# Performance work log

Measured on AMD Instinct MI355X. Metric: run time of the kernel, lower is better.

## Reference

```python
import jax, jax.numpy as jnp
import numpy as np
from jax import lax

B, L, DIM = 2, 2048, 2048
HK, HV = 16, 32
DK, DV = 128, 128
KCONV = 4
KEY_DIM = HK * DK          # 2048
VAL_DIM = HV * DV          # 4096
CONV_DIM = 2 * KEY_DIM + VAL_DIM  # 8192
EPS = 1e-6


def _l2norm(x, eps=1e-6):
    return x * lax.rsqrt((x * x).sum(-1, keepdims=True) + eps)


def _gated_delta_rule(q, k, v, g, beta):
    # q,k: (B,L,H,DK); v: (B,L,H,DV); g,beta: (B,L,H)
    q = _l2norm(q.astype(jnp.float32)) * (DK ** -0.5)
    k = _l2norm(k.astype(jnp.float32))
    v = v.astype(jnp.float32)
    g = g.astype(jnp.float32)
    beta = beta.astype(jnp.float32)
    # time-major for scan: (L,B,H,...)
    qs = q.transpose(1, 0, 2, 3)
    ks = k.transpose(1, 0, 2, 3)
    vs = v.transpose(1, 0, 2, 3)
    gs = g.transpose(1, 0, 2)
    bs = beta.transpose(1, 0, 2)
    state0 = jnp.zeros((B, HV, DK, DV), jnp.float32)

    def step(state, inp):
        q_t, k_t, v_t, g_t, b_t = inp
        state = state * jnp.exp(g_t)[..., None, None]          # decay
        kv_mem = jnp.einsum('bhk,bhkv->bhv', k_t, state)       # read
        delta = (v_t - kv_mem) * b_t[..., None]                # error-correct
        state = state + jnp.einsum('bhk,bhv->bhkv', k_t, delta)
        out_t = jnp.einsum('bhk,bhkv->bhv', q_t, state)
        return state, out_t

    _, outs = lax.scan(step, state0, (qs, ks, vs, gs, bs))
    return outs.transpose(1, 0, 2, 3)  # (B,L,H,DV)


def setup_inputs() -> dict:
    key = jax.random.key(0)
    ks = jax.random.split(key, 8)
    s = 0.02
    return {
        'x': jax.random.normal(ks[0], (B, L, DIM), jnp.float32),
        'W_qkv': jax.random.normal(ks[1], (CONV_DIM, DIM), jnp.float32) * s,
        'W_z': jax.random.normal(ks[2], (VAL_DIM, DIM), jnp.float32) * s,
        'W_a': jax.random.normal(ks[3], (HV, DIM), jnp.float32) * s,
        'W_b': jax.random.normal(ks[4], (HV, DIM), jnp.float32) * s,
        'conv_w': jax.random.normal(ks[5], (CONV_DIM, 1, KCONV), jnp.float32) * 0.2,
        'A_log': jnp.log(jax.random.uniform(ks[6], (HV,), jnp.float32, 1e-6, 16.0)),
        'dt_bias': jnp.ones((HV,), jnp.float32),
        'norm_weight': jnp.ones((DV,), jnp.float32),
        'W_out': jax.random.normal(ks[7], (DIM, VAL_DIM), jnp.float32) * s,
    }


def reference(x, W_qkv, W_z, W_a, W_b, conv_w, A_log, dt_bias, norm_weight, W_out):
    qkv = x @ W_qkv.T                      # (B,L,CONV_DIM)
    z = x @ W_z.T                          # (B,L,VAL_DIM)
    a = x @ W_a.T                          # (B,L,HV)
    b = x @ W_b.T                          # (B,L,HV)
    # depthwise causal conv1d (left pad K-1)
    h = qkv.transpose(0, 2, 1)             # (B,C,L)
    h = lax.conv_general_dilated(h, conv_w, window_strides=(1,),
                                 padding=[(KCONV - 1, 0)],
                                 dimension_numbers=('NCH', 'OIH', 'NCH'),
                                 feature_group_count=CONV_DIM)
    qkv = jax.nn.silu(h.transpose(0, 2, 1))
    q, k, v = jnp.split(qkv, [KEY_DIM, 2 * KEY_DIM], axis=-1)
    q = q.reshape(B, L, HK, DK)
    k = k.reshape(B, L, HK, DK)
    v = v.reshape(B, L, HV, DV)
    rep = HV // HK
    if rep > 1:
        q = jnp.repeat(q, rep, axis=2)
        k = jnp.repeat(k, rep, axis=2)
    g = -jnp.exp(A_log.astype(jnp.float32)) * jax.nn.softplus(a.astype(jnp.float32) + dt_bias)
    beta = jax.nn.sigmoid(b)
    out = _gated_delta_rule(q, k, v, g, beta)   # (B,L,HV,DV) fp32
    # gated RMSNorm over DV: silu(z) * weight * norm(out)
    var = (out * out).mean(-1, keepdims=True)
    out = out * lax.rsqrt(var + EPS) * norm_weight
    zg = z.reshape(B, L, HV, DV)
    out = out * jax.nn.silu(zg.astype(jnp.float32))
    out = out.astype(x.dtype).reshape(B, L, VAL_DIM)
    return out @ W_out.T
```

## Files before the change

### kernel.cpp

```cpp
#include <hip/hip_runtime.h>
#include <hip/hip_bf16.h>
#include <cstddef>
#include <cstdint>

constexpr int B = 2, L = 2048, DIM = 2048;
constexpr int HK = 16, HV = 32, DK = 128, DV = 128;
constexpr int KEY_DIM = HK * DK;
constexpr int VAL_DIM = HV * DV;
constexpr int CONV_DIM = 2 * KEY_DIM + VAL_DIM;
constexpr int NPROJ = CONV_DIM + VAL_DIM + HV + HV;
constexpr int NPAD  = ((NPROJ + 255) / 256) * 256;
constexpr size_t ROWS = (size_t)B * L;
constexpr float EPS = 1e-6f;
constexpr int CHUNK = 64, NCHUNK = L / CHUNK;
constexpr int NCH_TOT = B * HV * NCHUNK;
constexpr int CONV_LT = 8;
constexpr int CONV_TL = L / CONV_LT;

constexpr size_t OFF_QKV  = 0;
constexpr size_t OFF_Z    = OFF_QKV + ROWS * CONV_DIM * 2;
constexpr size_t OFF_A    = OFF_Z   + ROWS * VAL_DIM * 2;
constexpr size_t OFF_B    = OFF_A   + ROWS * HV * 4;
constexpr size_t OFF_G    = OFF_B   + ROWS * HV * 4;
constexpr size_t OFF_BETA = OFF_G   + ROWS * HV * 4;
constexpr size_t OFF_U    = OFF_BETA + ROWS * HV * 4;
constexpr size_t OFF_WQK  = OFF_U + (size_t)NCH_TOT * CHUNK * DV * 4;
constexpr size_t OFF_HALO = OFF_WQK + (size_t)NCH_TOT * CHUNK * CHUNK * 2;
constexpr size_t WS_NEED_BYTES = OFF_HALO + (size_t)3 * B * CONV_LT * CONV_DIM * 2;
constexpr size_t OFF_WCAT = OFF_U;
constexpr size_t OFF_XB   = OFF_WQK;
constexpr size_t OFF_WOB  = OFF_U;
static_assert((size_t)NPAD * DIM * 2 <= (size_t)NCH_TOT * CHUNK * DV * 4, "Wcat fits U");

__device__ __forceinline__ float bf2f(unsigned short u) {
    union { float f; uint32_t i; } c; c.i = ((uint32_t)u) << 16; return c.f;
}
__device__ __forceinline__ unsigned short f2bf(float f) {
    union { float f; uint32_t u; } c; c.f = f;
    uint32_t u = c.u + 0x7FFFu + ((c.u >> 16) & 1u);
    return (unsigned short)(u >> 16);
}
__device__ __forceinline__ uint32_t pk2(float a, float b) {
    return (uint32_t)f2bf(a) | ((uint32_t)f2bf(b) << 16);
}

typedef __attribute__((ext_vector_type(8))) short bfrag;
typedef __attribute__((ext_vector_type(4))) float ffrag;

__device__ __forceinline__ void gload16(const unsigned short* g, unsigned short* l) {
    __builtin_amdgcn_global_load_lds(
        (const __attribute__((address_space(1))) uint32_t*)g,
        (__attribute__((address_space(3))) uint32_t*)l, 16, 0, 0);
}

__device__ __forceinline__ const float* w_row_multi(int n, const float* Wq, const float* Wz,
                                                    const float* Wa, const float* Wb) {
    if (n < CONV_DIM)                return Wq + (size_t)n * DIM;
    if (n < CONV_DIM + VAL_DIM)      return Wz + (size_t)(n - CONV_DIM) * DIM;
    if (n < CONV_DIM + VAL_DIM + HV) return Wa + (size_t)(n - CONV_DIM - VAL_DIM) * DIM;
    return Wb + (size_t)(n - CONV_DIM - VAL_DIM - HV) * DIM;
}

__global__ __launch_bounds__(256) void cvt_wcat(
    const float* __restrict__ Wq, const float* __restrict__ Wz,
    const float* __restrict__ Wa, const float* __restrict__ Wb,
    unsigned short* __restrict__ dst)
{
    const int r = blockIdx.x;
    const int c = threadIdx.x * 8;
    uint4 o;
    if (r < NPROJ) {
        const float* s = w_row_multi(r, Wq, Wz, Wa, Wb) + c;
        float4 v0 = *(const float4*)s;
        float4 v1 = *(const float4*)(s + 4);
        o = make_uint4(pk2(v0.x, v0.y), pk2(v0.z, v0.w), pk2(v1.x, v1.y), pk2(v1.z, v1.w));
    } else {
        o = make_uint4(0u, 0u, 0u, 0u);
    }
    *(uint4*)&dst[(size_t)r * DIM + c] = o;
}

__global__ __launch_bounds__(256) void cvt_f32bf(const float* __restrict__ src,
                                                 unsigned short* __restrict__ dst, int cols)
{
    const size_t r = blockIdx.x;
    for (int c = threadIdx.x * 8; c < cols; c += 256 * 8) {
        const float* s = src + r * cols + c;
        float4 v0 = *(const float4*)s;
        float4 v1 = *(const float4*)(s + 4);
        *(uint4*)&dst[r * cols + c] =
            make_uint4(pk2(v0.x, v0.y), pk2(v0.z, v0.w), pk2(v1.x, v1.y), pk2(v1.z, v1.w));
    }
}

__device__ __forceinline__ void store_multi(int m, int n, float v,
                                            unsigned short* qkv, unsigned short* z,
                                            float* a, float* b) {
    if (n < CONV_DIM) {
        qkv[(size_t)m * CONV_DIM + n] = f2bf(v);
    } else if (n < CONV_DIM + VAL_DIM) {
        z[(size_t)m * VAL_DIM + (n - CONV_DIM)] = f2bf(v);
    } else if (n < CONV_DIM + VAL_DIM + HV) {
        a[(size_t)m * HV + (n - CONV_DIM - VAL_DIM)] = v;
    } else if (n < NPROJ) {
        b[(size_t)m * HV + (n - CONV_DIM - VAL_DIM - HV)] = v;
    }
}

constexpr int BK = 64;

constexpr int GBUF2 = 16384;
constexpr int GEMM_SMEM = 2 * GBUF2 * 2;

__global__ __launch_bounds__(256) void gemm_inproj_bf(
    const unsigned short* __restrict__ xb,
    const unsigned short* __restrict__ Wcat,
    unsigned short* __restrict__ qkv, unsigned short* __restrict__ z,
    float* __restrict__ a_out, float* __restrict__ b_out)
{
    extern __shared__ __align__(16) unsigned short lds[];

    constexpr int NT  = DIM / BK;
    constexpr int NBY = (int)ROWS / 128;
    constexpr int NBX = NPAD / 128;
    constexpr int NB  = NBY * NBX;
    const int id  = blockIdx.x;
    const int swz = (id & 7) * (NB >> 3) + (id >> 3);
    const int by  = swz & 31;
    const int bx  = swz >> 5;
    const int row0 = by * 128;
    const int col0 = bx * 128;

    const int t = threadIdx.x, lane = t & 63, wid = t >> 6;
    const int wm = (wid >> 1) * 64, wn = (wid & 1) * 64;
    const int quad = lane >> 4, l16 = lane & 15;
    const int x7 = l16 & 7;

    ffrag acc[4][4];
#pragma unroll
    for (int i = 0; i < 4; ++i)
#pragma unroll
        for (int j = 0; j < 4; ++j) acc[i][j] = (ffrag)0.f;

    const int srow = t >> 3;
    const int scol = (((t & 7) ^ (srow & 7)) * 8);
    const unsigned short* aS = xb   + (size_t)(row0 + srow) * DIM + scol;
    const unsigned short* bS = Wcat + (size_t)(col0 + srow) * DIM + scol;
    unsigned short* aD0 = lds + (wid * 8) * 64;
    unsigned short* bD0 = lds + 8192 + (wid * 8) * 64;

    auto STAGE = [&](int kt) {
        const int b = kt & 1;
        unsigned short* aD = aD0 + b * GBUF2;
        unsigned short* bD = bD0 + b * GBUF2;
        const int k0 = kt * BK;
#pragma unroll
        for (int g = 0; g < 4; ++g) {
            gload16(aS + (size_t)(g * 32) * DIM + k0, aD + g * 32 * 64);
            gload16(bS + (size_t)(g * 32) * DIM + k0, bD + g * 32 * 64);
        }
    };

    auto COMPUTE = [&](int kt) {
        const int b = kt & 1;
        const unsigned short* A  = lds + b * GBUF2;
        const unsigned short* Bm = lds + b * GBUF2 + 8192;
#pragma unroll
        for (int kk = 0; kk < 2; ++kk) {
            const int so = ((kk * 4 + quad) ^ x7) * 8;
            bfrag aF[4], bF[4];
#pragma unroll
            for (int m = 0; m < 4; ++m)
                aF[m] = *(const bfrag*)&A[(wm + m * 16 + l16) * 64 + so];
#pragma unroll
            for (int n = 0; n < 4; ++n)
                bF[n] = *(const bfrag*)&Bm[(wn + n * 16 + l16) * 64 + so];
            __builtin_amdgcn_s_setprio(1);
#pragma unroll
            for (int m = 0; m < 4; ++m)
#pragma unroll
                for (int n = 0; n < 4; ++n)
                    acc[m][n] = __builtin_amdgcn_mfma_f32_16x16x32_bf16(
                        aF[m], bF[n], acc[m][n], 0, 0, 0);
            __builtin_amdgcn_s_setprio(0);
        }
    };

    STAGE(0); STAGE(1);
    asm volatile("s_waitcnt vmcnt(8)" ::: "memory");
    asm volatile("s_barrier" ::: "memory");
    for (int kt = 0; kt < NT; ++kt) {
        COMPUTE(kt);
        if (kt == NT - 1) break;
        asm volatile("s_barrier" ::: "memory");
        if (kt + 2 < NT) {
            STAGE(kt + 2);
            asm volatile("s_waitcnt vmcnt(8)" ::: "memory");
        } else {
            asm volatile("s_waitcnt vmcnt(0)" ::: "memory");
        }
        asm volatile("s_barrier" ::: "memory");
    }

#pragma unroll
    for (int m = 0; m < 4; ++m)
#pragma unroll
        for (int n = 0; n < 4; ++n) {
            int gr = row0 + wm + m * 16 + quad * 4;
            int gc = col0 + wn + n * 16 + l16;
#pragma unroll
            for (int reg = 0; reg < 4; ++reg)
                store_multi(gr + reg, gc, acc[m][n][reg], qkv, z, a_out, b_out);
        }
}

constexpr int GBUF3 = 24576;
constexpr int GEMM3_SMEM = 3 * GBUF3 * 2;

__global__ __launch_bounds__(512, 1) void gemm_outproj_bf(
    const unsigned short* __restrict__ A,
    const unsigned short* __restrict__ Wb,
    float* __restrict__ C)
{
    extern __shared__ __align__(16) unsigned short lds[];

    constexpr int NT  = VAL_DIM / BK;
    constexpr int NBY = (int)ROWS / 256;
    constexpr int NBX = DIM / 128;
    constexpr int NB  = NBY * NBX;
    const int id  = blockIdx.x;
    const int swz = (id & 7) * (NB >> 3) + (id >> 3);
    const int by  = swz & 15;
    const int bx  = swz >> 4;
    const int row0 = by * 256;
    const int col0 = bx * 128;

    const int t = threadIdx.x, lane = t & 63, wid = t >> 6;
    const int wr = wid >> 1, wc = wid & 1;
    const int quad = lane >> 4, l16 = lane & 15;
    const int x7 = l16 & 7;

    ffrag acc[4][4];
#pragma unroll
    for (int i = 0; i < 4; ++i)
#pragma unroll
        for (int j = 0; j < 4; ++j) acc[i][j] = (ffrag)0.f;

    const int srow = t >> 3;
    const int scol = (((t & 7) ^ (srow & 7)) * 8);
    const unsigned short* aS = A  + (size_t)(row0 + srow) * VAL_DIM + scol;
    const unsigned short* bS = Wb + (size_t)(col0 + srow) * VAL_DIM + scol;
    unsigned short* aD0 = lds + (wid * 8) * 64;
    unsigned short* bD0 = lds + 16384 + (wid * 8) * 64;

    auto STAGE = [&](int kt) {
        const int b = kt % 3;
        unsigned short* aD = aD0 + b * GBUF3;
        unsigned short* bD = bD0 + b * GBUF3;
        const int k0 = kt * BK;
#pragma unroll
        for (int g = 0; g < 4; ++g)
            gload16(aS + (size_t)(g * 64) * VAL_DIM + k0, aD + g * 64 * 64);
#pragma unroll
        for (int g = 0; g < 2; ++g)
            gload16(bS + (size_t)(g * 64) * VAL_DIM + k0, bD + g * 64 * 64);
    };

    auto COMPUTE = [&](int kt) {
        const int b = kt % 3;
        const unsigned short* Am = lds + b * GBUF3;
        const unsigned short* Bm = lds + b * GBUF3 + 16384;
#pragma unroll
        for (int kk = 0; kk < 2; ++kk) {
            const int so = ((kk * 4 + quad) ^ x7) * 8;
            bfrag aF[4], bF[4];
#pragma unroll
            for (int m = 0; m < 4; ++m)
                aF[m] = *(const bfrag*)&Am[(wr * 64 + m * 16 + l16) * 64 + so];
#pragma unroll
            for (int n = 0; n < 4; ++n)
                bF[n] = *(const bfrag*)&Bm[(wc * 64 + n * 16 + l16) * 64 + so];
#pragma unroll
            for (int m = 0; m < 4; ++m)
#pragma unroll
                for (int n = 0; n < 4; ++n)
                    acc[m][n] = __builtin_amdgcn_mfma_f32_16x16x32_bf16(
                        aF[m], bF[n], acc[m][n], 0, 0, 0);
        }
    };

    STAGE(0); STAGE(1);
    asm volatile("s_waitcnt vmcnt(6)" ::: "memory");
    asm volatile("s_barrier" ::: "memory");
    for (int kt = 0; kt < NT; ++kt) {
        if (kt + 2 < NT) {
            STAGE(kt + 2);
            asm volatile("s_waitcnt vmcnt(12)" ::: "memory");
        } else if (kt + 1 < NT) {
            asm volatile("s_waitcnt vmcnt(6)" ::: "memory");
        } else {
            asm volatile("s_waitcnt vmcnt(0)" ::: "memory");
        }
        asm volatile("s_barrier" ::: "memory");
        COMPUTE(kt);
        asm volatile("s_barrier" ::: "memory");
    }

#pragma unroll
    for (int m = 0; m < 4; ++m)
#pragma unroll
        for (int n = 0; n < 4; ++n) {
            int gr = row0 + wr * 64 + m * 16 + quad * 4;
            int gc = col0 + wc * 64 + n * 16 + l16;
#pragma unroll
            for (int reg = 0; reg < 4; ++reg)
                C[(size_t)(gr + reg) * DIM + gc] = acc[m][n][reg];
        }
}

__global__ __launch_bounds__(256) void conv_halo(const unsigned short* __restrict__ qkv,
                                                 unsigned short* __restrict__ hbuf)
{
    int idx = blockIdx.x * 256 + threadIdx.x;
    int c    = idx & (CONV_DIM - 1);
    int tile = (idx >> 13) & (CONV_LT - 1);
    int b    = idx >> 16;
    int l0 = tile * CONV_TL;
    const unsigned short* p = qkv + (size_t)b * L * CONV_DIM + c;
#pragma unroll
    for (int j = 0; j < 3; ++j) {
        unsigned short v = (tile > 0) ? p[(size_t)(l0 - 3 + j) * CONV_DIM] : (unsigned short)0;
        hbuf[((size_t)j * B * CONV_LT + b * CONV_LT + tile) * CONV_DIM + c] = v;
    }
}

__global__ __launch_bounds__(256) void conv_silu(unsigned short* __restrict__ qkv,
                                                 const float* __restrict__ conv_w,
                                                 const unsigned short* __restrict__ hbuf)
{
    int idx = blockIdx.x * 256 + threadIdx.x;
    int c    = idx & (CONV_DIM - 1);
    int tile = (idx >> 13) & (CONV_LT - 1);
    int b    = idx >> 16;
    const float w0 = conv_w[c * 4 + 0];
    const float w1 = conv_w[c * 4 + 1];
    const float w2 = conv_w[c * 4 + 2];
    const float w3 = conv_w[c * 4 + 3];
    unsigned short* p = qkv + ((size_t)b * L + tile * CONV_TL) * CONV_DIM + c;
    const size_t hb = (size_t)b * CONV_LT + tile;
    float x0 = bf2f(hbuf[((size_t)0 * B * CONV_LT + hb) * CONV_DIM + c]);
    float x1 = bf2f(hbuf[((size_t)1 * B * CONV_LT + hb) * CONV_DIM + c]);
    float x2 = bf2f(hbuf[((size_t)2 * B * CONV_LT + hb) * CONV_DIM + c]);
    for (int l0 = 0; l0 < CONV_TL; l0 += 8) {
        float xv[8];
#pragma unroll
        for (int j = 0; j < 8; ++j) xv[j] = bf2f(p[(size_t)(l0 + j) * CONV_DIM]);
#pragma unroll
        for (int j = 0; j < 8; ++j) {
            float h = w0 * x0 + w1 * x1 + w2 * x2 + w3 * xv[j];
            float s = h / (1.f + __expf(-h));
            p[(size_t)(l0 + j) * CONV_DIM] = f2bf(s);
            x0 = x1; x1 = x2; x2 = xv[j];
        }
    }
}

__global__ __launch_bounds__(256) void normqk(unsigned short* __restrict__ qkv)
{
    int wid  = blockIdx.x * 4 + (threadIdx.x >> 6);
    int lane = threadIdx.x & 63;
    int hk  = wid & 15;
    int sel = (wid >> 4) & 1;
    int row = wid >> 5;
    unsigned short* p = qkv + (size_t)row * CONV_DIM + sel * KEY_DIM + hk * DK;
    float x0 = bf2f(p[lane]), x1 = bf2f(p[lane + 64]);
    float ss = x0 * x0 + x1 * x1;
#pragma unroll
    for (int o = 32; o >= 1; o >>= 1) ss += __shfl_xor(ss, o);
    float sc = rsqrtf(ss + 1e-6f);
    if (sel == 0) sc *= 0.08838834764831845f;
    p[lane]      = f2bf(x0 * sc);
    p[lane + 64] = f2bf(x1 * sc);
}

__global__ __launch_bounds__(256) void gatecoef(const float* __restrict__ a_buf,
                                                const float* __restrict__ b_buf,
                                                const float* __restrict__ A_log,
                                                const float* __restrict__ dt_bias,
                                                float* __restrict__ glog,
                                                float* __restrict__ beta)
{
    int idx = blockIdx.x * blockDim.x + threadIdx.x;
    int h = idx & (HV - 1);
    float av = a_buf[idx];
    float bv = b_buf[idx];
    float x  = av + dt_bias[h];
    float sp = (x > 20.f) ? x : log1pf(__expf(x));
    glog[idx] = -__expf(A_log[h]) * sp;
    beta[idx] = 1.f / (1.f + __expf(-bv));
}


constexpr int RSK  = 136;
constexpr int RST  = 72;
constexpr int RSTD = 68;
constexpr int RSR1 = 260;

constexpr int P1_oKs  = 0;
constexpr int P1_oQs  = P1_oKs + 64 * RSK * 2;
constexpr int P1_oDT  = 0;
constexpr int P1_oAf  = P1_oQs + 64 * RSK * 2;
constexpr int P1_oRHS = P1_oAf + 64 * RST * 2;
constexpr int P1_oG   = P1_oRHS + 64 * RSR1 * 4;
constexpr int P1_oEG  = P1_oG + 256;
constexpr int P1_oBs  = P1_oEG + 256;
constexpr int P1_SMEM = P1_oBs + 256;

__global__ __launch_bounds__(256, 1) void chunk_prep(
    unsigned short* __restrict__ qkv,
    const float* __restrict__ glog,
    const float* __restrict__ beta,
    float* __restrict__ Ubuf,
    unsigned short* __restrict__ Wqkbuf)
{
    extern __shared__ __align__(16) char smem[];
    unsigned short* sKs = (unsigned short*)(smem + P1_oKs);
    unsigned short* sQs = (unsigned short*)(smem + P1_oQs);
    unsigned short* sDT = (unsigned short*)(smem + P1_oDT);
    unsigned short* sAf = (unsigned short*)(smem + P1_oAf);
    float* sRHS = (float*)(smem + P1_oRHS);
    float* sG   = (float*)(smem + P1_oG);
    float* sEG  = (float*)(smem + P1_oEG);
    float* sBs  = (float*)(smem + P1_oBs);

    const int bid = blockIdx.x;
    const int ch = bid & (NCHUNK - 1);
    const int h  = (bid >> 5) & (HV - 1);
    const int bb = bid >> 10;
    const int hk = h >> 1;
    const int t    = threadIdx.x;
    const int w    = t >> 6;
    const int lane = t & 63;
    const int quad = lane >> 4;
    const int l16  = lane & 15;
    const int quad8 = quad * 8;
    const size_t bL = (size_t)bb * L;
    const int l0 = ch * CHUNK;
    const int VOFF = 2 * KEY_DIM + h * DV;

    {
        const int r  = t >> 2;
        const int c0 = (t & 3) * 32;
        const unsigned short* grow = qkv + (bL + l0 + r) * CONV_DIM;
        const unsigned short* gq = grow + hk * DK + c0;
        const unsigned short* gk = grow + KEY_DIM + hk * DK + c0;
#pragma unroll
        for (int u = 0; u < 4; ++u) {
            *(uint4*)&sKs[r * RSK + c0 + 8 * u] = *(const uint4*)(gk + 8 * u);
            *(uint4*)&sQs[r * RSK + c0 + 8 * u] = *(const uint4*)(gq + 8 * u);
        }
        if (t < 64) {
            float gl = glog[(bL + l0 + t) * HV + h];
#pragma unroll
            for (int off = 1; off < 64; off <<= 1) {
                float v = __shfl_up(gl, off, 64);
                if (lane >= off) gl += v;
            }
            sG[t]  = gl;
            sEG[t] = __expf(gl);
            sBs[t] = beta[(bL + l0 + t) * HV + h];
        }
    }
    __syncthreads();

    {
        ffrag accA[4], accW[4];
#pragma unroll
        for (int mt = 0; mt < 4; ++mt) { accA[mt] = (ffrag)0.f; accW[mt] = (ffrag)0.f; }
#pragma unroll
        for (int kk = 0; kk < 4; ++kk) {
            bfrag bf = *(const bfrag*)&sKs[(16 * w + l16) * RSK + 32 * kk + quad8];
#pragma unroll
            for (int mt = 0; mt < 4; ++mt) {
                bfrag ak = *(const bfrag*)&sKs[(16 * mt + l16) * RSK + 32 * kk + quad8];
                bfrag aq = *(const bfrag*)&sQs[(16 * mt + l16) * RSK + 32 * kk + quad8];
                accA[mt] = __builtin_amdgcn_mfma_f32_16x16x32_bf16(ak, bf, accA[mt], 0, 0, 0);
                accW[mt] = __builtin_amdgcn_mfma_f32_16x16x32_bf16(aq, bf, accW[mt], 0, 0, 0);
            }
        }
        const int j = 16 * w + l16;
        const float gj = sG[j];
        unsigned short* Wqp = Wqkbuf + (size_t)bid * (CHUNK * CHUNK);
#pragma unroll
        for (int mt = 0; mt < 4; ++mt)
#pragma unroll
            for (int reg = 0; reg < 4; ++reg) {
                int i = 16 * mt + quad * 4 + reg;
                float sc = __expf(sG[i] - gj);
                sAf[i * RST + j] = f2bf((j < i) ? sBs[i] * sc * accA[mt][reg] : 0.f);
                Wqp[i * CHUNK + j] = f2bf((j <= i) ? sc * accW[mt][reg] : 0.f);
            }
    }

    {
        const int r  = t >> 2;
        const int c0 = (t & 3) * 32;
        const float be  = sBs[r];
        const float beg = be * sEG[r];
        const unsigned short* gv = qkv + (bL + l0 + r) * CONV_DIM + VOFF + c0;
#pragma unroll
        for (int u = 0; u < 4; ++u) {
            uint4 vv = *(const uint4*)(gv + 8 * u);
            const unsigned short* vp = (const unsigned short*)&vv;
#pragma unroll
            for (int e = 0; e < 8; ++e)
                sRHS[r * RSR1 + c0 + 8 * u + e] = be * bf2f(vp[e]);
        }
#pragma unroll
        for (int u = 0; u < 4; ++u)
#pragma unroll
            for (int e = 0; e < 8; ++e)
                sRHS[r * RSR1 + 128 + c0 + 8 * u + e] =
                    beg * bf2f(sKs[r * RSK + c0 + 8 * u + e]);
    }
    __syncthreads();

    for (int u = t; u < 256 * RSTD / 2; u += 256) ((uint32_t*)sDT)[u] = 0;

    float* Up = Ubuf + (size_t)bid * (CHUNK * DV);
    for (int sb = 0; sb < 4; ++sb) {
        const int sb16 = 16 * sb;
        if (sb > 0) {
            const int kbn = (sb + 1) >> 1;
            ffrag c16[4];
#pragma unroll
            for (int nt = 0; nt < 4; ++nt) c16[nt] = (ffrag)0.f;
            for (int kb = 0; kb < kbn; ++kb) {
                bfrag af = *(const bfrag*)&sAf[(sb16 + l16) * RST + 32 * kb + quad8];
#pragma unroll
                for (int nt = 0; nt < 4; ++nt) {
                    bfrag bf = *(const bfrag*)&sDT[(64 * w + 16 * nt + l16) * RSTD + 32 * kb + quad8];
                    c16[nt] = __builtin_amdgcn_mfma_f32_16x16x32_bf16(af, bf, c16[nt], 0, 0, 0);
                }
            }
#pragma unroll
            for (int nt = 0; nt < 4; ++nt)
#pragma unroll
                for (int reg = 0; reg < 4; ++reg)
                    sRHS[(sb16 + quad * 4 + reg) * RSR1 + 64 * w + 16 * nt + l16] -= c16[nt][reg];
        }
        __syncthreads();
        {
            const int c = t;
            float d16[16];
#pragma unroll
            for (int e = 0; e < 16; ++e) {
                const int i = sb16 + e;
                float acc = sRHS[i * RSR1 + c];
#pragma unroll
                for (int f = 0; f < 16; ++f)
                    if (f < e) acc -= bf2f(sAf[i * RST + sb16 + f]) * d16[f];
                d16[e] = acc;
            }
#pragma unroll
            for (int e = 0; e < 16; e += 2)
                *(uint32_t*)&sDT[c * RSTD + sb16 + e] = pk2(d16[e], d16[e + 1]);
            if (c < 128) {
                float* up = Up + c;
#pragma unroll
                for (int e = 0; e < 16; ++e) up[(size_t)(sb16 + e) * DV] = d16[e];
            } else {
                unsigned short* wp = qkv + (bL + l0 + sb16) * CONV_DIM + VOFF + (c - 128);
#pragma unroll
                for (int e = 0; e < 16; ++e) wp[(size_t)e * CONV_DIM] = f2bf(-d16[e]);
            }
        }
        __syncthreads();
    }
}

constexpr int S3_oKT  = 0;
constexpr int S3_oQs  = S3_oKT + 128 * RST * 2;
constexpr int S3_oWk  = S3_oQs + 64 * RSK * 2;
constexpr int S3_oWqk = S3_oWk + 64 * RSK * 2;
constexpr int S3_oSTb = S3_oWqk + 64 * RST * 2;
constexpr int S3_oDT  = S3_oSTb + 32 * RSK * 2;
constexpr int S3_oDdT = S3_oDT + 32 * RST * 2;
constexpr int S3_oEG  = S3_oDdT + 32 * RST * 2;
constexpr int S3_oEGd = S3_oEG + 256;
constexpr int S3_SMEM = S3_oEGd + 256;

__global__ __launch_bounds__(256, 1) void chunk_scan3(
    const unsigned short* __restrict__ qkv,
    const float* __restrict__ glog,
    float* __restrict__ Ubuf,
    const unsigned short* __restrict__ Wqkbuf)
{
    extern __shared__ __align__(16) char smem[];
    unsigned short* sKT  = (unsigned short*)(smem + S3_oKT);
    unsigned short* sQs  = (unsigned short*)(smem + S3_oQs);
    unsigned short* sWk  = (unsigned short*)(smem + S3_oWk);
    unsigned short* sWqk = (unsigned short*)(smem + S3_oWqk);
    unsigned short* sSTb = (unsigned short*)(smem + S3_oSTb);
    unsigned short* sDT  = (unsigned short*)(smem + S3_oDT);
    unsigned short* sDdT = (unsigned short*)(smem + S3_oDdT);
    float* sEG  = (float*)(smem + S3_oEG);
    float* sEGd = (float*)(smem + S3_oEGd);

    const int g  = blockIdx.x & 3;
    const int bh = blockIdx.x >> 2;
    const int h  = bh & (HV - 1);
    const int bb = bh >> 5;
    const int hk = h >> 1;
    const int DV0 = g * 32;
    const int t    = threadIdx.x;
    const int w    = t >> 6;
    const int lane = t & 63;
    const int quad = lane >> 4;
    const int l16  = lane & 15;
    const int quad8 = quad * 8;
    const size_t bL = (size_t)bb * L;
    const int VOFF = 2 * KEY_DIM + h * DV;
    const size_t chbase0 = ((size_t)bb * HV + h) * NCHUNK;

    const int r  = t >> 2;
    const int c0 = (t & 3) * 32;
    const int cw = (t & 3) * 16;

    ffrag accS[2][2];
#pragma unroll
    for (int m = 0; m < 2; ++m)
#pragma unroll
        for (int n = 0; n < 2; ++n) accS[m][n] = (ffrag)0.f;

    for (int u = t; u < 32 * RSK / 2; u += 256) ((uint32_t*)sSTb)[u] = 0;

    uint4 pQ[4], pK[4], pWk[4], pWqk2[2];
    float pGl;

    auto PF = [&](int ch) {
        const int l0p = ch * CHUNK;
        const unsigned short* grow = qkv + (bL + l0p + r) * CONV_DIM;
        const unsigned short* gq = grow + hk * DK + c0;
        const unsigned short* gk = grow + KEY_DIM + hk * DK + c0;
        const unsigned short* gw = grow + VOFF + c0;
#pragma unroll
        for (int u = 0; u < 4; ++u) {
            pQ[u]  = *(const uint4*)(gq + 8 * u);
            pK[u]  = *(const uint4*)(gk + 8 * u);
            pWk[u] = *(const uint4*)(gw + 8 * u);
        }
        const unsigned short* qp = Wqkbuf + (chbase0 + ch) * (CHUNK * CHUNK) + r * CHUNK + cw;
        pWqk2[0] = *(const uint4*)qp;
        pWqk2[1] = *(const uint4*)(qp + 8);
        pGl = glog[(bL + l0p + (t & 63)) * HV + h];
    };

    PF(0);

    for (int ch = 0; ch < NCHUNK; ++ch) {
        const size_t cb = chbase0 + ch;
        float* Uch = Ubuf + cb * (CHUNK * DV);
        __syncthreads();

        ffrag accD[2];
        {
            const float* up = Uch + (size_t)(16 * w + quad * 4) * DV + DV0 + l16;
#pragma unroll
            for (int nt = 0; nt < 2; ++nt)
#pragma unroll
                for (int reg = 0; reg < 4; ++reg)
                    accD[nt][reg] = up[(size_t)reg * DV + 16 * nt];
        }

#pragma unroll
        for (int u = 0; u < 4; ++u) {
            *(uint4*)&sQs[r * RSK + c0 + 8 * u] = pQ[u];
            *(uint4*)&sWk[r * RSK + c0 + 8 * u] = pWk[u];
            const unsigned short* kp = (const unsigned short*)&pK[u];
#pragma unroll
            for (int e = 0; e < 8; ++e) {
                const int c = c0 + 8 * u + e;
                sKT[c * RST + ((((r >> 3) ^ (c >> 3)) & 7) << 3) + (r & 7)] = kp[e];
            }
        }
        *(uint4*)&sWqk[r * RST + cw]     = pWqk2[0];
        *(uint4*)&sWqk[r * RST + cw + 8] = pWqk2[1];

        {
            float gl = pGl;
            if (t < 64) {
#pragma unroll
                for (int off = 1; off < 64; off <<= 1) {
                    float v = __shfl_up(gl, off, 64);
                    if (lane >= off) gl += v;
                }
                float gc = __shfl(gl, 63, 64);
                sEG[t]  = __expf(gl);
                sEGd[t] = __expf(gc - gl);
            }
        }

        if (ch + 1 < NCHUNK) PF(ch + 1);
        __syncthreads();

#pragma unroll
        for (int kk = 0; kk < 4; ++kk) {
            bfrag af = *(const bfrag*)&sWk[(16 * w + l16) * RSK + 32 * kk + quad8];
#pragma unroll
            for (int nt = 0; nt < 2; ++nt) {
                bfrag bf = *(const bfrag*)&sSTb[(16 * nt + l16) * RSK + 32 * kk + quad8];
                accD[nt] = __builtin_amdgcn_mfma_f32_16x16x32_bf16(af, bf, accD[nt], 0, 0, 0);
            }
        }

        {
            const int i0 = 16 * w + quad * 4;
            const float e0 = sEGd[i0], e1 = sEGd[i0 + 1], e2 = sEGd[i0 + 2], e3 = sEGd[i0 + 3];
#pragma unroll
            for (int nt = 0; nt < 2; ++nt) {
                const int dv = 16 * nt + l16;
                const float d0 = accD[nt][0], d1 = accD[nt][1];
                const float d2 = accD[nt][2], d3 = accD[nt][3];
                *(uint32_t*)&sDT[dv * RST + i0]      = pk2(d0, d1);
                *(uint32_t*)&sDT[dv * RST + i0 + 2]  = pk2(d2, d3);
                *(uint32_t*)&sDdT[dv * RST + i0]     = pk2(d0 * e0, d1 * e1);
                *(uint32_t*)&sDdT[dv * RST + i0 + 2] = pk2(d2 * e2, d3 * e3);
            }
        }
        __syncthreads();

        ffrag accO[2];
#pragma unroll
        for (int nt = 0; nt < 2; ++nt) accO[nt] = (ffrag)0.f;
#pragma unroll
        for (int kk = 0; kk < 4; ++kk) {
            bfrag af = *(const bfrag*)&sQs[(16 * w + l16) * RSK + 32 * kk + quad8];
#pragma unroll
            for (int nt = 0; nt < 2; ++nt) {
                bfrag bf = *(const bfrag*)&sSTb[(16 * nt + l16) * RSK + 32 * kk + quad8];
                accO[nt] = __builtin_amdgcn_mfma_f32_16x16x32_bf16(af, bf, accO[nt], 0, 0, 0);
            }
        }
#pragma unroll
        for (int nt = 0; nt < 2; ++nt)
#pragma unroll
            for (int reg = 0; reg < 4; ++reg)
                accO[nt][reg] *= sEG[16 * w + quad * 4 + reg];
#pragma unroll
        for (int kk = 0; kk < 2; ++kk) {
            bfrag af = *(const bfrag*)&sWqk[(16 * w + l16) * RST + 32 * kk + quad8];
#pragma unroll
            for (int nt = 0; nt < 2; ++nt) {
                bfrag bf = *(const bfrag*)&sDT[(16 * nt + l16) * RST + 32 * kk + quad8];
                accO[nt] = __builtin_amdgcn_mfma_f32_16x16x32_bf16(af, bf, accO[nt], 0, 0, 0);
            }
        }
        {
            float* op = Uch + (size_t)(16 * w + quad * 4) * DV + DV0 + l16;
#pragma unroll
            for (int nt = 0; nt < 2; ++nt)
#pragma unroll
                for (int reg = 0; reg < 4; ++reg)
                    op[(size_t)reg * DV + 16 * nt] = accO[nt][reg];
        }

        {
            const float eGc = sEG[63];
#pragma unroll
            for (int m = 0; m < 2; ++m)
#pragma unroll
                for (int n = 0; n < 2; ++n)
#pragma unroll
                    for (int reg = 0; reg < 4; ++reg) accS[m][n][reg] *= eGc;
#pragma unroll
            for (int kk = 0; kk < 2; ++kk) {
#pragma unroll
                for (int m = 0; m < 2; ++m) {
                    bfrag a0 = *(const bfrag*)&sDdT[(16 * m + l16) * RST + 32 * kk + quad8];
#pragma unroll
                    for (int n = 0; n < 2; ++n) {
                        const int ck = 32 * w + 16 * n + l16;
                        bfrag bk = *(const bfrag*)&sKT[ck * RST +
                                     ((((4 * kk + quad) ^ (ck >> 3)) & 7) << 3)];
                        accS[m][n] = __builtin_amdgcn_mfma_f32_16x16x32_bf16(a0, bk, accS[m][n], 0, 0, 0);
                    }
                }
            }
        }
        __syncthreads();

#pragma unroll
        for (int m = 0; m < 2; ++m)
#pragma unroll
            for (int n = 0; n < 2; ++n)
#pragma unroll
                for (int reg = 0; reg < 4; ++reg)
                    sSTb[(16 * m + quad * 4 + reg) * RSK + 32 * w + 16 * n + l16] =
                        f2bf(accS[m][n][reg]);
    }
}

__global__ __launch_bounds__(256) void rmsgate(
    const float* __restrict__ Obuf,
    unsigned short* __restrict__ z_io,
    const float* __restrict__ norm_w)
{
    const int gw   = blockIdx.x * 4 + (threadIdx.x >> 6);
    const int lane = threadIdx.x & 63;
    const int h  = gw & (HV - 1);
    const int lg = gw >> 5;
    const int bb = lg >> 11;
    const int l  = lg & (L - 1);
    const int ch = l >> 6, i = l & 63;
    const size_t cb = ((size_t)bb * HV + h) * NCHUNK + ch;
    const int dv0 = lane * 2;

    float2 o = *(const float2*)(Obuf + cb * (CHUNK * DV) + (size_t)i * DV + dv0);
    float p = o.x * o.x + o.y * o.y;
#pragma unroll
    for (int m = 1; m < 64; m <<= 1) p += __shfl_xor(p, m, 64);
    float inv = rsqrtf(p * (1.f / 128.f) + EPS);

    unsigned short* zp = z_io + ((size_t)bb * L + l) * VAL_DIM + h * DV + dv0;
    uint32_t zu = *(const uint32_t*)zp;
    float z0 = bf2f((unsigned short)(zu & 0xFFFF));
    float z1 = bf2f((unsigned short)(zu >> 16));
    float y0 = o.x * inv * norm_w[dv0]     * (z0 / (1.f + __expf(-z0)));
    float y1 = o.y * inv * norm_w[dv0 + 1] * (z1 / (1.f + __expf(-z1)));
    *(uint32_t*)zp = pk2(y0, y1);
}

extern "C" void kernel_launch(void* const* d_in, const int* in_sizes, int n_in,
                              void* d_out, int out_size, void* d_ws, size_t ws_size,
                              hipStream_t stream)
{
    const float* x        = (const float*)d_in[0];
    const float* W_qkv    = (const float*)d_in[1];
    const float* W_z      = (const float*)d_in[2];
    const float* W_a      = (const float*)d_in[3];
    const float* W_b      = (const float*)d_in[4];
    const float* conv_w   = (const float*)d_in[5];
    const float* A_log    = (const float*)d_in[6];
    const float* dt_bias  = (const float*)d_in[7];
    const float* norm_w   = (const float*)d_in[8];
    const float* W_out    = (const float*)d_in[9];
    float* out = (float*)d_out;
    char*  ws  = (char*)d_ws;

    if (ws_size < WS_NEED_BYTES) return;

    unsigned short* qkv = (unsigned short*)(ws + OFF_QKV);
    unsigned short* z   = (unsigned short*)(ws + OFF_Z);
    float* a    = (float*)(ws + OFF_A);
    float* bbuf = (float*)(ws + OFF_B);
    float* gl   = (float*)(ws + OFF_G);
    float* beta = (float*)(ws + OFF_BETA);
    float* Ubuf = (float*)(ws + OFF_U);
    unsigned short* Wqkbuf = (unsigned short*)(ws + OFF_WQK);
    unsigned short* hbuf   = (unsigned short*)(ws + OFF_HALO);
    unsigned short* Wcat   = (unsigned short*)(ws + OFF_WCAT);
    unsigned short* xb     = (unsigned short*)(ws + OFF_XB);
    unsigned short* Wob    = (unsigned short*)(ws + OFF_WOB);

    static bool attr_set = false;
    if (!attr_set) {
        (void)hipFuncSetAttribute((const void*)chunk_prep,
                                  hipFuncAttributeMaxDynamicSharedMemorySize, P1_SMEM);
        (void)hipFuncSetAttribute((const void*)chunk_scan3,
                                  hipFuncAttributeMaxDynamicSharedMemorySize, S3_SMEM);
        (void)hipFuncSetAttribute((const void*)gemm_inproj_bf,
                                  hipFuncAttributeMaxDynamicSharedMemorySize, GEMM_SMEM);
        (void)hipFuncSetAttribute((const void*)gemm_outproj_bf,
                                  hipFuncAttributeMaxDynamicSharedMemorySize, GEMM3_SMEM);
        attr_set = true;
    }

    cvt_wcat<<<NPAD, 256, 0, stream>>>(W_qkv, W_z, W_a, W_b, Wcat);
    cvt_f32bf<<<(int)ROWS, 256, 0, stream>>>(x, xb, DIM);
    gemm_inproj_bf<<<((int)ROWS / 128) * (NPAD / 128), 256, GEMM_SMEM, stream>>>(
        xb, Wcat, qkv, z, a, bbuf);
    conv_halo<<<(B * CONV_LT * CONV_DIM) / 256, 256, 0, stream>>>(qkv, hbuf);
    conv_silu<<<(B * CONV_LT * CONV_DIM) / 256, 256, 0, stream>>>(qkv, conv_w, hbuf);
    normqk<<<(B * L * 2 * HK) / 4, 256, 0, stream>>>(qkv);
    gatecoef<<<(B * L * HV) / 256, 256, 0, stream>>>(a, bbuf, A_log, dt_bias, gl, beta);
    chunk_prep<<<NCH_TOT, 256, P1_SMEM, stream>>>(qkv, gl, beta, Ubuf, Wqkbuf);
    chunk_scan3<<<B * HV * 4, 256, S3_SMEM, stream>>>(qkv, gl, Ubuf, Wqkbuf);
    rmsgate<<<(int)(ROWS * HV) / 4, 256, 0, stream>>>(Ubuf, z, norm_w);
    cvt_f32bf<<<DIM, 256, 0, stream>>>(W_out, Wob, VAL_DIM);
    gemm_outproj_bf<<<((int)ROWS / 256) * (DIM / 128), 512, GEMM3_SMEM, stream>>>(z, Wob, out);
}
```

Baseline: 880.8 us.

## Shrink GEMM K-tile to 32 and retile out-projection to 128x128 blocks

Both projection GEMMs now use a 32-wide K tile with a double-buffered 32 KB LDS footprint and a new 4-way XOR swizzle. The out-projection drops from 256x128 tiles with 512 threads and triple buffering to 128x128 tiles with 256 threads, matching the in-projection pipeline. The smaller LDS use should let more blocks reside per CU for better latency hiding and give more blocks for the out-projection. In exchange there are twice as many K iterations and barriers, and each tile gets less data reuse.

```diff
diff --git a/kernel.cpp b/kernel.cpp
--- a/kernel.cpp
+++ b/kernel.cpp
@@ -107,10 +107,10 @@
     }
 }
 
-constexpr int BK = 64;
-
-constexpr int GBUF2 = 16384;
-constexpr int GEMM_SMEM = 2 * GBUF2 * 2;
+constexpr int BK32  = 32;
+constexpr int GBUFA = 4096;
+constexpr int GBUFP = 8192;
+constexpr int GEMM_SMEM32 = 2 * GBUFP * 2;
 
 __global__ __launch_bounds__(256) void gemm_inproj_bf(
     const unsigned short* __restrict__ xb,
@@ -120,7 +120,7 @@
 {
     extern __shared__ __align__(16) unsigned short lds[];
 
-    constexpr int NT  = DIM / BK;
+    constexpr int NT  = DIM / BK32;
     constexpr int NBY = (int)ROWS / 128;
     constexpr int NBX = NPAD / 128;
     constexpr int NB  = NBY * NBX;
@@ -134,7 +134,6 @@
     const int t = threadIdx.x, lane = t & 63, wid = t >> 6;
     const int wm = (wid >> 1) * 64, wn = (wid & 1) * 64;
     const int quad = lane >> 4, l16 = lane & 15;
-    const int x7 = l16 & 7;
 
     ffrag acc[4][4];
 #pragma unroll
@@ -142,52 +141,50 @@
 #pragma unroll
         for (int j = 0; j < 4; ++j) acc[i][j] = (ffrag)0.f;
 
-    const int srow = t >> 3;
-    const int scol = (((t & 7) ^ (srow & 7)) * 8);
-    const unsigned short* aS = xb   + (size_t)(row0 + srow) * DIM + scol;
-    const unsigned short* bS = Wcat + (size_t)(col0 + srow) * DIM + scol;
-    unsigned short* aD0 = lds + (wid * 8) * 64;
-    unsigned short* bD0 = lds + 8192 + (wid * 8) * 64;
+    const int srow = wid * 32 + (lane >> 2);
+    const int scol = (((lane & 3) ^ ((lane >> 2) & 3)) * 8);
+    const unsigned short* aS0 = xb   + (size_t)(row0 + srow) * DIM + scol;
+    const unsigned short* aS1 = aS0 + (size_t)16 * DIM;
+    const unsigned short* bS0 = Wcat + (size_t)(col0 + srow) * DIM + scol;
+    const unsigned short* bS1 = bS0 + (size_t)16 * DIM;
+    unsigned short* aD = lds + wid * 1024;
+    unsigned short* bD = lds + GBUFA + wid * 1024;
 
     auto STAGE = [&](int kt) {
         const int b = kt & 1;
-        unsigned short* aD = aD0 + b * GBUF2;
-        unsigned short* bD = bD0 + b * GBUF2;
-        const int k0 = kt * BK;
-#pragma unroll
-        for (int g = 0; g < 4; ++g) {
-            gload16(aS + (size_t)(g * 32) * DIM + k0, aD + g * 32 * 64);
-            gload16(bS + (size_t)(g * 32) * DIM + k0, bD + g * 32 * 64);
-        }
+        const int k0 = kt * BK32;
+        unsigned short* a  = aD + b * GBUFP;
+        unsigned short* bb = bD + b * GBUFP;
+        gload16(aS0 + k0, a);
+        gload16(aS1 + k0, a + 512);
+        gload16(bS0 + k0, bb);
+        gload16(bS1 + k0, bb + 512);
     };
 
     auto COMPUTE = [&](int kt) {
         const int b = kt & 1;
-        const unsigned short* A  = lds + b * GBUF2;
-        const unsigned short* Bm = lds + b * GBUF2 + 8192;
-#pragma unroll
-        for (int kk = 0; kk < 2; ++kk) {
-            const int so = ((kk * 4 + quad) ^ x7) * 8;
-            bfrag aF[4], bF[4];
-#pragma unroll
-            for (int m = 0; m < 4; ++m)
-                aF[m] = *(const bfrag*)&A[(wm + m * 16 + l16) * 64 + so];
+        const unsigned short* A  = lds + b * GBUFP;
+        const unsigned short* Bm = A + GBUFA;
+        const int so = ((quad ^ (l16 & 3)) << 3);
+        bfrag aF[4], bF[4];
+#pragma unroll
+        for (int m = 0; m < 4; ++m)
+            aF[m] = *(const bfrag*)&A[(wm + m * 16 + l16) * 32 + so];
+#pragma unroll
+        for (int n = 0; n < 4; ++n)
+            bF[n] = *(const bfrag*)&Bm[(wn + n * 16 + l16) * 32 + so];
+        __builtin_amdgcn_s_setprio(1);
+#pragma unroll
+        for (int m = 0; m < 4; ++m)
 #pragma unroll
             for (int n = 0; n < 4; ++n)
-                bF[n] = *(const bfrag*)&Bm[(wn + n * 16 + l16) * 64 + so];
-            __builtin_amdgcn_s_setprio(1);
-#pragma unroll
-            for (int m = 0; m < 4; ++m)
-#pragma unroll
-                for (int n = 0; n < 4; ++n)
-                    acc[m][n] = __builtin_amdgcn_mfma_f32_16x16x32_bf16(
-                        aF[m], bF[n], acc[m][n], 0, 0, 0);
-            __builtin_amdgcn_s_setprio(0);
-        }
+                acc[m][n] = __builtin_amdgcn_mfma_f32_16x16x32_bf16(
+                    aF[m], bF[n], acc[m][n], 0, 0, 0);
+        __builtin_amdgcn_s_setprio(0);
     };
 
     STAGE(0); STAGE(1);
-    asm volatile("s_waitcnt vmcnt(8)" ::: "memory");
+    asm volatile("s_waitcnt vmcnt(4)" ::: "memory");
     asm volatile("s_barrier" ::: "memory");
     for (int kt = 0; kt < NT; ++kt) {
         COMPUTE(kt);
@@ -195,7 +192,7 @@
         asm volatile("s_barrier" ::: "memory");
         if (kt + 2 < NT) {
             STAGE(kt + 2);
-            asm volatile("s_waitcnt vmcnt(8)" ::: "memory");
+            asm volatile("s_waitcnt vmcnt(4)" ::: "memory");
         } else {
             asm volatile("s_waitcnt vmcnt(0)" ::: "memory");
         }
@@ -214,31 +211,27 @@
         }
 }
 
-constexpr int GBUF3 = 24576;
-constexpr int GEMM3_SMEM = 3 * GBUF3 * 2;
-
-__global__ __launch_bounds__(512, 1) void gemm_outproj_bf(
+__global__ __launch_bounds__(256) void gemm_outproj_bf(
     const unsigned short* __restrict__ A,
     const unsigned short* __restrict__ Wb,
     float* __restrict__ C)
 {
     extern __shared__ __align__(16) unsigned short lds[];
 
-    constexpr int NT  = VAL_DIM / BK;
-    constexpr int NBY = (int)ROWS / 256;
+    constexpr int NT  = VAL_DIM / BK32;
+    constexpr int NBY = (int)ROWS / 128;
     constexpr int NBX = DIM / 128;
     constexpr int NB  = NBY * NBX;
     const int id  = blockIdx.x;
     const int swz = (id & 7) * (NB >> 3) + (id >> 3);
-    const int by  = swz & 15;
-    const int bx  = swz >> 4;
-    const int row0 = by * 256;
+    const int by  = swz & 31;
+    const int bx  = swz >> 5;
+    const int row0 = by * 128;
     const int col0 = bx * 128;
 
     const int t = threadIdx.x, lane = t & 63, wid = t >> 6;
-    const int wr = wid >> 1, wc = wid & 1;
+    const int wm = (wid >> 1) * 64, wn = (wid & 1) * 64;
     const int quad = lane >> 4, l16 = lane & 15;
-    const int x7 = l16 & 7;
 
     ffrag acc[4][4];
 #pragma unroll
@@ -246,72 +239,70 @@
 #pragma unroll
         for (int j = 0; j < 4; ++j) acc[i][j] = (ffrag)0.f;
 
-    const int srow = t >> 3;
-    const int scol = (((t & 7) ^ (srow & 7)) * 8);
-    const unsigned short* aS = A  + (size_t)(row0 + srow) * VAL_DIM + scol;
-    const unsigned short* bS = Wb + (size_t)(col0 + srow) * VAL_DIM + scol;
-    unsigned short* aD0 = lds + (wid * 8) * 64;
-    unsigned short* bD0 = lds + 16384 + (wid * 8) * 64;
+    const int srow = wid * 32 + (lane >> 2);
+    const int scol = (((lane & 3) ^ ((lane >> 2) & 3)) * 8);
+    const unsigned short* aS0 = A  + (size_t)(row0 + srow) * VAL_DIM + scol;
+    const unsigned short* aS1 = aS0 + (size_t)16 * VAL_DIM;
+    const unsigned short* bS0 = Wb + (size_t)(col0 + srow) * VAL_DIM + scol;
+    const unsigned short* bS1 = bS0 + (size_t)16 * VAL_DIM;
+    unsigned short* aD = lds + wid * 1024;
+    unsigned short* bD = lds + GBUFA + wid * 1024;
 
     auto STAGE = [&](int kt) {
-        const int b = kt % 3;
-        unsigned short* aD = aD0 + b * GBUF3;
-        unsigned short* bD = bD0 + b * GBUF3;
-        const int k0 = kt * BK;
-#pragma unroll
-        for (int g = 0; g < 4; ++g)
-            gload16(aS + (size_t)(g * 64) * VAL_DIM + k0, aD + g * 64 * 64);
-#pragma unroll
-        for (int g = 0; g < 2; ++g)
-            gload16(bS + (size_t)(g * 64) * VAL_DIM + k0, bD + g * 64 * 64);
+        const int b = kt & 1;
+        const int k0 = kt * BK32;
+        unsigned short* a  = aD + b * GBUFP;
+        unsigned short* bb = bD + b * GBUFP;
+        gload16(aS0 + k0, a);
+        gload16(aS1 + k0, a + 512);
+        gload16(bS0 + k0, bb);
+        gload16(bS1 + k0, bb + 512);
     };
 
     auto COMPUTE = [&](int kt) {
-        const int b = kt % 3;
-        const unsigned short* Am = lds + b * GBUF3;
-        const unsigned short* Bm = lds + b * GBUF3 + 16384;
-#pragma unroll
-        for (int kk = 0; kk < 2; ++kk) {
-            const int so = ((kk * 4 + quad) ^ x7) * 8;
-            bfrag aF[4], bF[4];
-#pragma unroll
-            for (int m = 0; m < 4; ++m)
-                aF[m] = *(const bfrag*)&Am[(wr * 64 + m * 16 + l16) * 64 + so];
+        const int b = kt & 1;
+        const unsigned short* Am = lds + b * GBUFP;
+        const unsigned short* Bm = Am + GBUFA;
+        const int so = ((quad ^ (l16 & 3)) << 3);
+        bfrag aF[4], bF[4];
+#pragma unroll
+        for (int m = 0; m < 4; ++m)
+            aF[m] = *(const bfrag*)&Am[(wm + m * 16 + l16) * 32 + so];
+#pragma unroll
+        for (int n = 0; n < 4; ++n)
+            bF[n] = *(const bfrag*)&Bm[(wn + n * 16 + l16) * 32 + so];
+        __builtin_amdgcn_s_setprio(1);
+#pragma unroll
+        for (int m = 0; m < 4; ++m)
 #pragma unroll
             for (int n = 0; n < 4; ++n)
-                bF[n] = *(const bfrag*)&Bm[(wc * 64 + n * 16 + l16) * 64 + so];
-#pragma unroll
-            for (int m = 0; m < 4; ++m)
-#pragma unroll
-                for (int n = 0; n < 4; ++n)
-                    acc[m][n] = __builtin_amdgcn_mfma_f32_16x16x32_bf16(
-                        aF[m], bF[n], acc[m][n], 0, 0, 0);
-        }
+                acc[m][n] = __builtin_amdgcn_mfma_f32_16x16x32_bf16(
+                    aF[m], bF[n], acc[m][n], 0, 0, 0);
+        __builtin_amdgcn_s_setprio(0);
     };
 
     STAGE(0); STAGE(1);
-    asm volatile("s_waitcnt vmcnt(6)" ::: "memory");
+    asm volatile("s_waitcnt vmcnt(4)" ::: "memory");
     asm volatile("s_barrier" ::: "memory");
     for (int kt = 0; kt < NT; ++kt) {
+        COMPUTE(kt);
+        if (kt == NT - 1) break;
+        asm volatile("s_barrier" ::: "memory");
         if (kt + 2 < NT) {
             STAGE(kt + 2);
-            asm volatile("s_waitcnt vmcnt(12)" ::: "memory");
-        } else if (kt + 1 < NT) {
-            asm volatile("s_waitcnt vmcnt(6)" ::: "memory");
+            asm volatile("s_waitcnt vmcnt(4)" ::: "memory");
         } else {
             asm volatile("s_waitcnt vmcnt(0)" ::: "memory");
         }
         asm volatile("s_barrier" ::: "memory");
-        COMPUTE(kt);
-        asm volatile("s_barrier" ::: "memory");
     }
 
 #pragma unroll
     for (int m = 0; m < 4; ++m)
 #pragma unroll
         for (int n = 0; n < 4; ++n) {
-            int gr = row0 + wr * 64 + m * 16 + quad * 4;
-            int gc = col0 + wc * 64 + n * 16 + l16;
+            int gr = row0 + wm + m * 16 + quad * 4;
+            int gc = col0 + wn + n * 16 + l16;
 #pragma unroll
             for (int reg = 0; reg < 4; ++reg)
                 C[(size_t)(gr + reg) * DIM + gc] = acc[m][n][reg];
@@ -870,15 +861,15 @@
         (void)hipFuncSetAttribute((const void*)chunk_scan3,
                                   hipFuncAttributeMaxDynamicSharedMemorySize, S3_SMEM);
         (void)hipFuncSetAttribute((const void*)gemm_inproj_bf,
-                                  hipFuncAttributeMaxDynamicSharedMemorySize, GEMM_SMEM);
+                                  hipFuncAttributeMaxDynamicSharedMemorySize, GEMM_SMEM32);
         (void)hipFuncSetAttribute((const void*)gemm_outproj_bf,
-                                  hipFuncAttributeMaxDynamicSharedMemorySize, GEMM3_SMEM);
+                                  hipFuncAttributeMaxDynamicSharedMemorySize, GEMM_SMEM32);
         attr_set = true;
     }
 
     cvt_wcat<<<NPAD, 256, 0, stream>>>(W_qkv, W_z, W_a, W_b, Wcat);
     cvt_f32bf<<<(int)ROWS, 256, 0, stream>>>(x, xb, DIM);
-    gemm_inproj_bf<<<((int)ROWS / 128) * (NPAD / 128), 256, GEMM_SMEM, stream>>>(
+    gemm_inproj_bf<<<((int)ROWS / 128) * (NPAD / 128), 256, GEMM_SMEM32, stream>>>(
         xb, Wcat, qkv, z, a, bbuf);
     conv_halo<<<(B * CONV_LT * CONV_DIM) / 256, 256, 0, stream>>>(qkv, hbuf);
     conv_silu<<<(B * CONV_LT * CONV_DIM) / 256, 256, 0, stream>>>(qkv, conv_w, hbuf);
@@ -888,5 +879,5 @@
     chunk_scan3<<<B * HV * 4, 256, S3_SMEM, stream>>>(qkv, gl, Ubuf, Wqkbuf);
     rmsgate<<<(int)(ROWS * HV) / 4, 256, 0, stream>>>(Ubuf, z, norm_w);
     cvt_f32bf<<<DIM, 256, 0, stream>>>(W_out, Wob, VAL_DIM);
-    gemm_outproj_bf<<<((int)ROWS / 256) * (DIM / 128), 512, GEMM3_SMEM, stream>>>(z, Wob, out);
-}
+    gemm_outproj_bf<<<((int)ROWS / 128) * (DIM / 128), 256, GEMM_SMEM32, stream>>>(z, Wob, out);
+}
```

Result: slower. 907.9 us (+3.1%).
